# Kernel tuning notes

Hardware: AMD Instinct MI355X
Metric: run time of the kernel (lower is better)

Reference implementation:

```python
import jax, jax.numpy as jnp
import numpy as np
from jax import lax

V, H, A, S = 256, 2048, 512, 512  # vocab, hidden, attn, seq_len


def setup_inputs() -> dict:
    key = jax.random.key(0)
    ks = jax.random.split(key, 8)
    sc = 0.02  # small init to keep tanh unsaturated
    return {
        "x_enc": jax.random.normal(ks[0], (S, V), jnp.float32),
        "x_dec": jax.random.normal(ks[1], (S, V), jnp.float32),
        "W_enc": jax.random.normal(ks[2], (H, V + H), jnp.float32) * sc,
        "b_enc": jnp.zeros((H,), jnp.float32),
        "Wa_enc": jax.random.normal(ks[3], (A, H), jnp.float32) * sc,
        "Wa_dec": jax.random.normal(ks[4], (A, H), jnp.float32) * sc,
        "v_a": jax.random.normal(ks[5], (A,), jnp.float32) * sc,
        "W_dec": jax.random.normal(ks[6], (H, V + 2 * H), jnp.float32) * sc,
        "b_dec": jnp.zeros((H,), jnp.float32),
        "W_out": jax.random.normal(ks[7], (V, H), jnp.float32) * sc,
        "b_out": jnp.zeros((V,), jnp.float32),
    }


def reference(x_enc, x_dec, W_enc, b_enc, Wa_enc, Wa_dec, v_a, W_dec, b_dec, W_out, b_out):
    h0 = jnp.zeros((W_enc.shape[0],), x_enc.dtype)

    # Encoder: h_t = tanh(W_enc [x_t ; h_{t-1}] + b)
    def enc_step(h, x):
        h_new = jnp.tanh(jnp.concatenate([x, h]) @ W_enc.T + b_enc)
        return h_new, h_new

    h_enc, enc_states = lax.scan(enc_step, h0, x_enc)  # enc_states: (S, H)

    # Encoder-side attention projection is step-invariant -> hoist (same math).
    enc_proj = enc_states @ Wa_enc.T  # (S, A)

    # Decoder with per-step Bahdanau additive attention.
    def dec_step(h, x):
        dec_proj = h @ Wa_dec.T                              # (A,)
        energy = jnp.tanh(enc_proj + dec_proj) @ v_a         # (S,)
        attn_w = jax.nn.softmax(energy)                      # (S,)
        context = attn_w @ enc_states                        # (H,)
        h_new = jnp.tanh(jnp.concatenate([x, context, h]) @ W_dec.T + b_dec)
        logits = h_new @ W_out.T + b_out                     # (V,)
        return h_new, logits

    _, outputs = lax.scan(dec_step, h_enc, x_dec)  # (S, V)
    return outputs
```

## Files before the change

kernel.cpp:

```cpp
#include <hip/hip_runtime.h>

#define V 256
#define H 2048
#define A 512
#define S 512

__global__ __launch_bounds__(256) void gemm_nt(
    const float* __restrict__ Amat, int lda,
    const float* __restrict__ Bmat, int ldb,
    float* __restrict__ C, int ldc,
    const float* __restrict__ bias, int M, int N, int K)
{
    __shared__ float As[16][68];
    __shared__ float Bs[16][68];
    const int tid = threadIdx.x;
    const int tx = tid & 15;
    const int ty = tid >> 4;
    const int m0 = blockIdx.y * 64;
    const int n0 = blockIdx.x * 64;
    const int lr = tid >> 2;
    const int lk = (tid & 3) * 4;

    float acc[4][4] = {};
    for (int k0 = 0; k0 < K; k0 += 16) {
        float4 av = *(const float4*)(Amat + (size_t)(m0 + lr) * lda + k0 + lk);
        float4 bv = *(const float4*)(Bmat + (size_t)(n0 + lr) * ldb + k0 + lk);
        __syncthreads();
        As[lk+0][lr] = av.x; As[lk+1][lr] = av.y; As[lk+2][lr] = av.z; As[lk+3][lr] = av.w;
        Bs[lk+0][lr] = bv.x; Bs[lk+1][lr] = bv.y; Bs[lk+2][lr] = bv.z; Bs[lk+3][lr] = bv.w;
        __syncthreads();
        #pragma unroll
        for (int k = 0; k < 16; ++k) {
            float a4[4], b4[4];
            #pragma unroll
            for (int i = 0; i < 4; ++i) a4[i] = As[k][ty*4+i];
            #pragma unroll
            for (int j = 0; j < 4; ++j) b4[j] = Bs[k][tx*4+j];
            #pragma unroll
            for (int i = 0; i < 4; ++i)
                #pragma unroll
                for (int j = 0; j < 4; ++j) acc[i][j] += a4[i] * b4[j];
        }
    }
    #pragma unroll
    for (int i = 0; i < 4; ++i) {
        const int m = m0 + ty*4 + i;
        #pragma unroll
        for (int j = 0; j < 4; ++j) {
            const int n = n0 + tx*4 + j;
            float v = acc[i][j];
            if (bias) v += bias[n];
            C[(size_t)m * ldc + n] = v;
        }
    }
}

__global__ __launch_bounds__(256) void enc_step(
    const float* __restrict__ W_enc,
    const float* __restrict__ accx,
    const float* __restrict__ h_prev,
    float* __restrict__ h_out, int t)
{
    const int wave = threadIdx.x >> 6;
    const int lane = threadIdx.x & 63;
    const int row  = blockIdx.x * 4 + wave;
    float acc = 0.f;
    if (t > 0) {
        const float4* w4 = (const float4*)(W_enc + (size_t)row * (V + H) + V);
        const float4* h4 = (const float4*)h_prev;
        #pragma unroll
        for (int it = 0; it < H/256; ++it) {
            float4 w = w4[lane + it*64];
            float4 hh = h4[lane + it*64];
            acc += w.x*hh.x + w.y*hh.y + w.z*hh.z + w.w*hh.w;
        }
    }
    for (int off = 32; off; off >>= 1) acc += __shfl_down(acc, off);
    if (lane == 0) h_out[row] = tanhf(acc + accx[row]);
}

__global__ __launch_bounds__(256) void dec_p1(
    const float* __restrict__ Wa_dec,
    const float* __restrict__ W_dec,
    const float* __restrict__ h_prev,
    float* __restrict__ dec_proj, float* __restrict__ acc_h)
{
    const int wave = threadIdx.x >> 6;
    const int lane = threadIdx.x & 63;
    const int r    = blockIdx.x * 4 + wave;
    const float* wr = (r < A) ? (Wa_dec + (size_t)r * H)
                              : (W_dec + (size_t)(r - A) * (V + 2*H) + V + H);
    const float4* w4 = (const float4*)wr;
    const float4* h4 = (const float4*)h_prev;
    float acc = 0.f;
    #pragma unroll
    for (int it = 0; it < H/256; ++it) {
        float4 w = w4[lane + it*64];
        float4 hh = h4[lane + it*64];
        acc += w.x*hh.x + w.y*hh.y + w.z*hh.z + w.w*hh.w;
    }
    for (int off = 32; off; off >>= 1) acc += __shfl_down(acc, off);
    if (lane == 0) { if (r < A) dec_proj[r] = acc; else acc_h[r - A] = acc; }
}

__global__ __launch_bounds__(256) void dec_p2(
    const float* __restrict__ enc_proj,
    const float* __restrict__ dec_proj,
    const float* __restrict__ v_a,
    float* __restrict__ e)
{
    const int wave = threadIdx.x >> 6;
    const int lane = threadIdx.x & 63;
    const int s    = blockIdx.x * 4 + wave;
    const float4* ep = (const float4*)(enc_proj + (size_t)s * A);
    const float4* dp = (const float4*)dec_proj;
    const float4* va = (const float4*)v_a;
    float acc = 0.f;
    #pragma unroll
    for (int it = 0; it < A/256; ++it) {
        float4 p = ep[lane + it*64];
        float4 d = dp[lane + it*64];
        float4 v = va[lane + it*64];
        acc += tanhf(p.x+d.x)*v.x + tanhf(p.y+d.y)*v.y + tanhf(p.z+d.z)*v.z + tanhf(p.w+d.w)*v.w;
    }
    for (int off = 32; off; off >>= 1) acc += __shfl_down(acc, off);
    if (lane == 0) e[s] = expf(acc);
}

__global__ __launch_bounds__(256) void dec_p3(
    const float* __restrict__ WcT,
    const float* __restrict__ e,
    const float* __restrict__ accx,
    const float* __restrict__ acc_h,
    float* __restrict__ h_out)
{
    __shared__ __align__(16) float es[S];
    __shared__ float zred[4];
    const int tid  = threadIdx.x;
    const int wave = tid >> 6;
    const int lane = tid & 63;

    float part = 0.f;
    for (int s = tid; s < S; s += 256) { float v = e[s]; es[s] = v; part += v; }
    for (int off = 32; off; off >>= 1) part += __shfl_down(part, off);
    if (lane == 0) zred[wave] = part;
    __syncthreads();
    const float Zinv = 1.f / (zred[0] + zred[1] + zred[2] + zred[3]);

    const int row = blockIdx.x * 4 + wave;
    const float4* w4 = (const float4*)(WcT + (size_t)row * S);
    const float4* e4 = (const float4*)es;
    float acc = 0.f;
    #pragma unroll
    for (int it = 0; it < S/256; ++it) {
        float4 w = w4[lane + it*64];
        float4 ev = e4[lane + it*64];
        acc += w.x*ev.x + w.y*ev.y + w.z*ev.z + w.w*ev.w;
    }
    for (int off = 32; off; off >>= 1) acc += __shfl_down(acc, off);
    if (lane == 0) h_out[row] = tanhf(accx[row] + acc_h[row] + acc * Zinv);
}

extern "C" void kernel_launch(void* const* d_in, const int* in_sizes, int n_in,
                              void* d_out, int out_size, void* d_ws, size_t ws_size,
                              hipStream_t stream) {
    const float* x_enc  = (const float*)d_in[0];
    const float* x_dec  = (const float*)d_in[1];
    const float* W_enc  = (const float*)d_in[2];
    const float* b_enc  = (const float*)d_in[3];
    const float* Wa_enc = (const float*)d_in[4];
    const float* Wa_dec = (const float*)d_in[5];
    const float* v_a    = (const float*)d_in[6];
    const float* W_dec  = (const float*)d_in[7];
    const float* b_dec  = (const float*)d_in[8];
    const float* W_out  = (const float*)d_in[9];
    const float* b_out  = (const float*)d_in[10];
    float* out = (float*)d_out;

    float* ws         = (float*)d_ws;
    float* accx_enc   = ws;
    float* enc_states = accx_enc + (size_t)S*H;
    float* enc_proj   = enc_states + (size_t)S*H;
    float* WcT        = enc_proj + (size_t)S*A;
    float* accx_dec   = WcT + (size_t)H*S;
    float* h_dec      = accx_dec + (size_t)S*H;
    float* dec_proj   = h_dec + (size_t)S*H;
    float* acc_h      = dec_proj + A;
    float* evec       = acc_h + H;

    dim3 b256(256);

    gemm_nt<<<dim3(H/64, S/64), b256, 0, stream>>>(x_enc, V, W_enc, V+H, accx_enc, H, b_enc, S, H, V);

    for (int t = 0; t < S; ++t) {
        enc_step<<<dim3(H/4), b256, 0, stream>>>(
            W_enc, accx_enc + (size_t)t*H,
            t ? enc_states + (size_t)(t-1)*H : accx_enc ,
            enc_states + (size_t)t*H, t);
    }

    gemm_nt<<<dim3(A/64, S/64), b256, 0, stream>>>(enc_states, H, Wa_enc, H, enc_proj, A, nullptr, S, A, H);

    gemm_nt<<<dim3(S/64, H/64), b256, 0, stream>>>(W_dec + V, V+2*H, enc_states, H, WcT, S, nullptr, H, S, H);

    gemm_nt<<<dim3(H/64, S/64), b256, 0, stream>>>(x_dec, V, W_dec, V+2*H, accx_dec, H, b_dec, S, H, V);

    for (int t = 0; t < S; ++t) {
        const float* hp = t ? h_dec + (size_t)(t-1)*H : enc_states + (size_t)(S-1)*H;
        dec_p1<<<dim3((A+H)/4), b256, 0, stream>>>(Wa_dec, W_dec, hp, dec_proj, acc_h);
        dec_p2<<<dim3(S/4),     b256, 0, stream>>>(enc_proj, dec_proj, v_a, evec);
        dec_p3<<<dim3(H/4),     b256, 0, stream>>>(WcT, evec, accx_dec + (size_t)t*H, acc_h, h_dec + (size_t)t*H);
    }

    gemm_nt<<<dim3(V/64, S/64), b256, 0, stream>>>(h_dec, H, W_out, H, out, V, b_out, S, V, H);
}
```

Baseline: 7.032 ms.

## Replace per-step kernel launches with persistent cooperative scan kernels using grid barriers

The encoder and decoder recurrences, previously 512 and 1536 small kernel launches, become one persistent cooperative kernel each. Each kernel has 256 blocks of 8 waves, and a software grid barrier built on atomics separates the dependent phases of each timestep. The decoder also fuses the Wa_dec and W_dec hidden-state matvecs into one pass and copies the hidden state, projections and attention weights into shared memory. This removes launch overhead and inter-kernel gaps, at the cost of spin-wait barrier latency and the requirement that all 256 blocks be co-resident.

Measured after the change: 27.93 ms. 3.97x slower.

```diff
diff --git a/kernel.cpp b/kernel.cpp
--- a/kernel.cpp
+++ b/kernel.cpp
@@ -4,6 +4,30 @@
 #define H 2048
 #define A 512
 #define S 512
+#define NBLK 256
+#define NTHR 512
+
+__device__ __forceinline__ void grid_barrier(int* cnt, int* sense, int* epoch_io) {
+    __syncthreads();
+    if (threadIdx.x == 0) {
+        const int e = ++(*epoch_io);
+        __threadfence();
+        int prev = __hip_atomic_fetch_add(cnt, 1, __ATOMIC_ACQ_REL, __HIP_MEMORY_SCOPE_AGENT);
+        if (prev == NBLK - 1) {
+            __hip_atomic_store(cnt, 0, __ATOMIC_RELAXED, __HIP_MEMORY_SCOPE_AGENT);
+            __hip_atomic_store(sense, e, __ATOMIC_RELEASE, __HIP_MEMORY_SCOPE_AGENT);
+        } else {
+            while (__hip_atomic_load(sense, __ATOMIC_RELAXED, __HIP_MEMORY_SCOPE_AGENT) < e)
+                __builtin_amdgcn_s_sleep(2);
+        }
+        __threadfence();
+    }
+    __syncthreads();
+}
+
+__global__ void init_bar(int* bar) {
+    bar[0] = 0; bar[64] = 0; bar[128] = 0; bar[192] = 0;
+}
 
 __global__ __launch_bounds__(256) void gemm_nt(
     const float* __restrict__ Amat, int lda,
@@ -55,110 +79,137 @@
     }
 }
 
-__global__ __launch_bounds__(256) void enc_step(
-    const float* __restrict__ W_enc,
-    const float* __restrict__ accx,
-    const float* __restrict__ h_prev,
-    float* __restrict__ h_out, int t)
+__global__ __launch_bounds__(NTHR, 1) void enc_scan(
+    const float* __restrict__ W_enc, const float* __restrict__ accx,
+    float* __restrict__ states, int* cnt, int* sense)
 {
-    const int wave = threadIdx.x >> 6;
-    const int lane = threadIdx.x & 63;
-    const int row  = blockIdx.x * 4 + wave;
-    float acc = 0.f;
-    if (t > 0) {
-        const float4* w4 = (const float4*)(W_enc + (size_t)row * (V + H) + V);
-        const float4* h4 = (const float4*)h_prev;
-        #pragma unroll
-        for (int it = 0; it < H/256; ++it) {
-            float4 w = w4[lane + it*64];
+    __shared__ __align__(16) float hs[H];
+    const int tid = threadIdx.x;
+    const int wid = tid >> 6, lane = tid & 63;
+    const int row = blockIdx.x * 8 + wid;
+    const float4* w4 = (const float4*)(W_enc + (size_t)row * (V + H) + V);
+    int epoch = 0;
+
+    if (lane == 0) states[row] = tanhf(accx[row]);
+
+    for (int t = 1; t < S; ++t) {
+        grid_barrier(cnt, sense, &epoch);
+        ((float4*)hs)[tid] = ((const float4*)(states + (size_t)(t-1)*H))[tid];
+        __syncthreads();
+        const float4* h4 = (const float4*)hs;
+        float acc = 0.f;
+        #pragma unroll
+        for (int it = 0; it < 8; ++it) {
+            float4 w  = w4[lane + it*64];
             float4 hh = h4[lane + it*64];
             acc += w.x*hh.x + w.y*hh.y + w.z*hh.z + w.w*hh.w;
         }
-    }
-    for (int off = 32; off; off >>= 1) acc += __shfl_down(acc, off);
-    if (lane == 0) h_out[row] = tanhf(acc + accx[row]);
-}
-
-__global__ __launch_bounds__(256) void dec_p1(
-    const float* __restrict__ Wa_dec,
-    const float* __restrict__ W_dec,
-    const float* __restrict__ h_prev,
-    float* __restrict__ dec_proj, float* __restrict__ acc_h)
+        #pragma unroll
+        for (int off = 32; off; off >>= 1) acc += __shfl_down(acc, off);
+        if (lane == 0) states[(size_t)t*H + row] = tanhf(acc + accx[(size_t)t*H + row]);
+    }
+}
+
+__global__ __launch_bounds__(NTHR, 1) void dec_scan(
+    const float* __restrict__ Wa_dec, const float* __restrict__ W_dec,
+    const float* __restrict__ enc_proj, const float* __restrict__ v_a,
+    const float* __restrict__ WcT, const float* __restrict__ accx,
+    const float* __restrict__ enc_states, float* __restrict__ h_dec,
+    float* __restrict__ dec_proj, float* __restrict__ evec,
+    int* cnt, int* sense)
 {
-    const int wave = threadIdx.x >> 6;
-    const int lane = threadIdx.x & 63;
-    const int r    = blockIdx.x * 4 + wave;
-    const float* wr = (r < A) ? (Wa_dec + (size_t)r * H)
-                              : (W_dec + (size_t)(r - A) * (V + 2*H) + V + H);
-    const float4* w4 = (const float4*)wr;
-    const float4* h4 = (const float4*)h_prev;
-    float acc = 0.f;
-    #pragma unroll
-    for (int it = 0; it < H/256; ++it) {
-        float4 w = w4[lane + it*64];
-        float4 hh = h4[lane + it*64];
-        acc += w.x*hh.x + w.y*hh.y + w.z*hh.z + w.w*hh.w;
-    }
-    for (int off = 32; off; off >>= 1) acc += __shfl_down(acc, off);
-    if (lane == 0) { if (r < A) dec_proj[r] = acc; else acc_h[r - A] = acc; }
-}
-
-__global__ __launch_bounds__(256) void dec_p2(
-    const float* __restrict__ enc_proj,
-    const float* __restrict__ dec_proj,
-    const float* __restrict__ v_a,
-    float* __restrict__ e)
-{
-    const int wave = threadIdx.x >> 6;
-    const int lane = threadIdx.x & 63;
-    const int s    = blockIdx.x * 4 + wave;
-    const float4* ep = (const float4*)(enc_proj + (size_t)s * A);
-    const float4* dp = (const float4*)dec_proj;
-    const float4* va = (const float4*)v_a;
-    float acc = 0.f;
-    #pragma unroll
-    for (int it = 0; it < A/256; ++it) {
-        float4 p = ep[lane + it*64];
-        float4 d = dp[lane + it*64];
-        float4 v = va[lane + it*64];
-        acc += tanhf(p.x+d.x)*v.x + tanhf(p.y+d.y)*v.y + tanhf(p.z+d.z)*v.z + tanhf(p.w+d.w)*v.w;
-    }
-    for (int off = 32; off; off >>= 1) acc += __shfl_down(acc, off);
-    if (lane == 0) e[s] = expf(acc);
-}
-
-__global__ __launch_bounds__(256) void dec_p3(
-    const float* __restrict__ WcT,
-    const float* __restrict__ e,
-    const float* __restrict__ accx,
-    const float* __restrict__ acc_h,
-    float* __restrict__ h_out)
-{
+    __shared__ __align__(16) float hs[H];
+    __shared__ __align__(16) float ps[A];
+    __shared__ __align__(16) float vs[A];
     __shared__ __align__(16) float es[S];
-    __shared__ float zred[4];
-    const int tid  = threadIdx.x;
-    const int wave = tid >> 6;
-    const int lane = tid & 63;
-
-    float part = 0.f;
-    for (int s = tid; s < S; s += 256) { float v = e[s]; es[s] = v; part += v; }
-    for (int off = 32; off; off >>= 1) part += __shfl_down(part, off);
-    if (lane == 0) zred[wave] = part;
-    __syncthreads();
-    const float Zinv = 1.f / (zred[0] + zred[1] + zred[2] + zred[3]);
-
-    const int row = blockIdx.x * 4 + wave;
-    const float4* w4 = (const float4*)(WcT + (size_t)row * S);
-    const float4* e4 = (const float4*)es;
-    float acc = 0.f;
-    #pragma unroll
-    for (int it = 0; it < S/256; ++it) {
-        float4 w = w4[lane + it*64];
-        float4 ev = e4[lane + it*64];
-        acc += w.x*ev.x + w.y*ev.y + w.z*ev.z + w.w*ev.w;
-    }
-    for (int off = 32; off; off >>= 1) acc += __shfl_down(acc, off);
-    if (lane == 0) h_out[row] = tanhf(accx[row] + acc_h[row] + acc * Zinv);
+    __shared__ float zred[8];
+    const int tid = threadIdx.x;
+    const int wid = tid >> 6, lane = tid & 63;
+    const int gw  = blockIdx.x * 8 + wid;
+    int epoch = 0;
+
+    if (tid < A/4) ((float4*)vs)[tid] = ((const float4*)v_a)[tid];
+
+    const float4* wd4 = (const float4*)(W_dec + (size_t)gw * (V + 2*H) + V + H);
+    const float4* wa4 = (const float4*)(Wa_dec + (size_t)gw * H);
+    const float4* wc4 = (const float4*)(WcT + (size_t)gw * S);
+
+    for (int t = 0; t < S; ++t) {
+        const float* hsrc = t ? (h_dec + (size_t)(t-1)*H) : (enc_states + (size_t)(S-1)*H);
+        ((float4*)hs)[tid] = ((const float4*)hsrc)[tid];
+        __syncthreads();
+
+        const float4* h4 = (const float4*)hs;
+        float accH = 0.f, accP = 0.f;
+        if (gw < A) {
+            #pragma unroll
+            for (int it = 0; it < 8; ++it) {
+                float4 hh = h4[lane + it*64];
+                float4 w  = wd4[lane + it*64];
+                float4 wa = wa4[lane + it*64];
+                accH += w.x*hh.x + w.y*hh.y + w.z*hh.z + w.w*hh.w;
+                accP += wa.x*hh.x + wa.y*hh.y + wa.z*hh.z + wa.w*hh.w;
+            }
+        } else {
+            #pragma unroll
+            for (int it = 0; it < 8; ++it) {
+                float4 hh = h4[lane + it*64];
+                float4 w  = wd4[lane + it*64];
+                accH += w.x*hh.x + w.y*hh.y + w.z*hh.z + w.w*hh.w;
+            }
+        }
+        #pragma unroll
+        for (int off = 32; off; off >>= 1) {
+            accH += __shfl_down(accH, off);
+            accP += __shfl_down(accP, off);
+        }
+        if (gw < A && lane == 0) dec_proj[gw] = accP;
+        grid_barrier(cnt, sense, &epoch);
+
+        if (tid < A/4) ((float4*)ps)[tid] = ((const float4*)dec_proj)[tid];
+        __syncthreads();
+        if (gw < S) {
+            const float4* ep4 = (const float4*)(enc_proj + (size_t)gw * A);
+            float e_ = 0.f;
+            #pragma unroll
+            for (int it = 0; it < 2; ++it) {
+                float4 p  = ep4[lane + it*64];
+                float4 d  = ((const float4*)ps)[lane + it*64];
+                float4 vv = ((const float4*)vs)[lane + it*64];
+                e_ += tanhf(p.x+d.x)*vv.x + tanhf(p.y+d.y)*vv.y
+                    + tanhf(p.z+d.z)*vv.z + tanhf(p.w+d.w)*vv.w;
+            }
+            #pragma unroll
+            for (int off = 32; off; off >>= 1) e_ += __shfl_down(e_, off);
+            if (lane == 0) evec[gw] = expf(e_);
+        }
+        grid_barrier(cnt, sense, &epoch);
+
+        if (tid < S/4) ((float4*)es)[tid] = ((const float4*)evec)[tid];
+        __syncthreads();
+        float z = es[tid];
+        #pragma unroll
+        for (int off = 32; off; off >>= 1) z += __shfl_down(z, off);
+        if (lane == 0) zred[wid] = z;
+        __syncthreads();
+        float Z = 0.f;
+        #pragma unroll
+        for (int i = 0; i < 8; ++i) Z += zred[i];
+        const float Zinv = 1.f / Z;
+
+        float ctx = 0.f;
+        #pragma unroll
+        for (int it = 0; it < 2; ++it) {
+            float4 w  = wc4[lane + it*64];
+            float4 ee = ((const float4*)es)[lane + it*64];
+            ctx += w.x*ee.x + w.y*ee.y + w.z*ee.z + w.w*ee.w;
+        }
+        #pragma unroll
+        for (int off = 32; off; off >>= 1) ctx += __shfl_down(ctx, off);
+        if (lane == 0)
+            h_dec[(size_t)t*H + gw] = tanhf(accx[(size_t)t*H + gw] + accH + ctx * Zinv);
+        grid_barrier(cnt, sense, &epoch);
+    }
 }
 
 extern "C" void kernel_launch(void* const* d_in, const int* in_sizes, int n_in,
@@ -185,31 +236,33 @@
     float* accx_dec   = WcT + (size_t)H*S;
     float* h_dec      = accx_dec + (size_t)S*H;
     float* dec_proj   = h_dec + (size_t)S*H;
-    float* acc_h      = dec_proj + A;
-    float* evec       = acc_h + H;
+    float* evec       = dec_proj + A;
+    int*   bar        = (int*)(evec + S);
+    int* cnt_e = bar,        * sen_e = bar + 64;
+    int* cnt_d = bar + 128,  * sen_d = bar + 192;
 
     dim3 b256(256);
 
+    init_bar<<<1, 1, 0, stream>>>(bar);
+
     gemm_nt<<<dim3(H/64, S/64), b256, 0, stream>>>(x_enc, V, W_enc, V+H, accx_enc, H, b_enc, S, H, V);
-
-    for (int t = 0; t < S; ++t) {
-        enc_step<<<dim3(H/4), b256, 0, stream>>>(
-            W_enc, accx_enc + (size_t)t*H,
-            t ? enc_states + (size_t)(t-1)*H : accx_enc ,
-            enc_states + (size_t)t*H, t);
+    gemm_nt<<<dim3(H/64, S/64), b256, 0, stream>>>(x_dec, V, W_dec, V+2*H, accx_dec, H, b_dec, S, H, V);
+
+    {
+        const float* We = W_enc; const float* ax = accx_enc; float* st = enc_states;
+        void* args[] = { &We, &ax, &st, &cnt_e, &sen_e };
+        hipLaunchCooperativeKernel((void*)enc_scan, dim3(NBLK), dim3(NTHR), args, 0, stream);
     }
 
     gemm_nt<<<dim3(A/64, S/64), b256, 0, stream>>>(enc_states, H, Wa_enc, H, enc_proj, A, nullptr, S, A, H);
-
     gemm_nt<<<dim3(S/64, H/64), b256, 0, stream>>>(W_dec + V, V+2*H, enc_states, H, WcT, S, nullptr, H, S, H);
 
-    gemm_nt<<<dim3(H/64, S/64), b256, 0, stream>>>(x_dec, V, W_dec, V+2*H, accx_dec, H, b_dec, S, H, V);
-
-    for (int t = 0; t < S; ++t) {
-        const float* hp = t ? h_dec + (size_t)(t-1)*H : enc_states + (size_t)(S-1)*H;
-        dec_p1<<<dim3((A+H)/4), b256, 0, stream>>>(Wa_dec, W_dec, hp, dec_proj, acc_h);
-        dec_p2<<<dim3(S/4),     b256, 0, stream>>>(enc_proj, dec_proj, v_a, evec);
-        dec_p3<<<dim3(H/4),     b256, 0, stream>>>(WcT, evec, accx_dec + (size_t)t*H, acc_h, h_dec + (size_t)t*H);
+    {
+        const float* wa = Wa_dec; const float* wd = W_dec; const float* ep = enc_proj;
+        const float* va = v_a; const float* wc = WcT; const float* ax = accx_dec;
+        const float* es = enc_states; float* hd = h_dec; float* dp = dec_proj; float* ev = evec;
+        void* args[] = { &wa, &wd, &ep, &va, &wc, &ax, &es, &hd, &dp, &ev, &cnt_d, &sen_d };
+        hipLaunchCooperativeKernel((void*)dec_scan, dim3(NBLK), dim3(NTHR), args, 0, stream);
     }
 
     gemm_nt<<<dim3(V/64, S/64), b256, 0, stream>>>(h_dec, H, W_out, H, out, V, b_out, S, V, H);
```
